# Performance work log

Hardware: AMD Instinct MI355X
Metric: run time of the kernel (lower is better)

Reference implementation:

```python
import jax, jax.numpy as jnp
import numpy as np

SIZE = 512  # context size
T, D1, D2 = 32768, 512, 512
HID = int(SIZE * 1.5)  # 768, units of the 'context_linear' Dense


def setup_inputs() -> dict:
    key = jax.random.key(0)
    ks = jax.random.split(key, 8)
    din = D1 + D2
    return {
        "x1": jax.random.normal(ks[0], (T, D1), jnp.float32),
        "x2": jax.random.normal(ks[1], (T, D2), jnp.float32),
        "context0": jax.random.normal(ks[2], (1, SIZE), jnp.float32) * 0.1,  # tf.Variable init stddev=0.1
        "W_linear": jax.random.normal(ks[3], (din, HID), jnp.float32) * 0.02,
        "b_linear": jnp.zeros((HID,), jnp.float32),
        "W_embed": jax.random.normal(ks[4], (HID, SIZE), jnp.float32) * 0.02,
        "W_rate": jax.random.normal(ks[5], (SIZE, 1), jnp.float32) * 0.02,
        "W_forget": jax.random.normal(ks[6], (SIZE, SIZE), jnp.float32) * 0.02,
    }


def reference(x1, x2, context0, W_linear, b_linear, W_embed, W_rate, W_forget):
    # z = embed(linear(concat(inputs))) : Dense(1.5*size, linear) -> Dense(size, sigmoid, no bias)
    z = jnp.concatenate([x1, x2], axis=-1)                      # [T, D1+D2]
    z = jax.nn.sigmoid((z @ W_linear + b_linear) @ W_embed)     # [T, SIZE]
    # rate gate depends only on z_t, so precompute it in one GEMM
    r = jnp.tanh(z @ W_rate)[:, 0]                              # [T]

    # recurrence: c_t = softmax(c_{t-1} @ Wf) * c_{t-1} + r_t * z_t
    def step(c, zr):
        zt, rt = zr
        f = jax.nn.softmax(c @ W_forget)                        # [SIZE]
        c_new = f * c + rt * zt
        return c_new, c_new

    _, ys = jax.lax.scan(step, context0[0], (z, r))             # ys: [T, SIZE]
    return ys
```

## Files before the change

### kernel.cpp

```cpp
#include <hip/hip_runtime.h>
#include <stdint.h>
#include <stddef.h>


typedef __attribute__((ext_vector_type(8))) short bf16x8;
typedef __attribute__((ext_vector_type(4))) float f32x4;

__device__ __forceinline__ unsigned short f32_to_bf16(float f) {
  union { float f; unsigned u; } v; v.f = f;
  unsigned u = v.u;
  return (unsigned short)((u + 0x7fffu + ((u >> 16) & 1u)) >> 16);
}
__device__ __forceinline__ float bf16_to_f32(unsigned short h) {
  union { unsigned u; float f; } v; v.u = ((unsigned)h) << 16; return v.f;
}

__device__ __forceinline__ unsigned char f32_to_e4m3(float f) {
  float a = fabsf(f);
  unsigned char s = (unsigned char)((__float_as_uint(f) >> 24) & 0x80u);
  if (a >= 448.0f) return s | 0x7Eu;
  if (a < 0.015625f) {
    unsigned m = (unsigned)rintf(a * 512.0f);
    return s | (unsigned char)m;
  }
  unsigned u = __float_as_uint(a);
  unsigned r = u + 0x7FFFFu + ((u >> 20) & 1u);
  unsigned e = (r >> 23) - 120u;
  unsigned m = (r >> 20) & 7u;
  if (e >= 16u) return s | 0x7Eu;
  return s | (unsigned char)((e << 3) | m);
}

__global__ void k_convert_x(const float* __restrict__ x1, const float* __restrict__ x2,
                            unsigned short* __restrict__ Xb) {
  int id = blockIdx.x * 256 + threadIdx.x;
  int t  = id >> 8;
  int c4 = (id & 255) * 4;
  float4 v;
  if (c4 < 512) v = *(const float4*)(x1 + (size_t)t * 512 + c4);
  else          v = *(const float4*)(x2 + (size_t)t * 512 + (c4 - 512));
  ushort4 o;
  o.x = f32_to_bf16(v.x); o.y = f32_to_bf16(v.y);
  o.z = f32_to_bf16(v.z); o.w = f32_to_bf16(v.w);
  *(ushort4*)(Xb + (size_t)t * 1024 + c4) = o;
}

__global__ void k_convert_w(const float* __restrict__ Wl, const float* __restrict__ We,
                            const float* __restrict__ Wf,
                            unsigned short* __restrict__ WlT, unsigned short* __restrict__ WeT,
                            unsigned char* __restrict__ Wf8) {
  int id = blockIdx.x * 256 + threadIdx.x;
  if (id < 786432) {
    int n = id >> 10, k = id & 1023;
    WlT[id] = f32_to_bf16(Wl[(size_t)k * 768 + n]);
  } else if (id < 1179648) {
    int j = id - 786432;
    int n = j / 768, k = j - n * 768;
    WeT[j] = f32_to_bf16(We[(size_t)k * 512 + n]);
  } else {
    int j = id - 1179648;
    int n = j >> 9, k = j & 511;
    Wf8[j] = f32_to_e4m3(Wf[(size_t)k * 512 + n] * 16.0f);
  }
}

template <int MODE>
__global__ void k_gemm_bt(const unsigned short* __restrict__ A,
                          const unsigned short* __restrict__ Bt,
                          const float* __restrict__ bias,
                          unsigned short* __restrict__ Cb,
                          float* __restrict__ Cf,
                          int M, int N, int K) {
  __shared__ unsigned short As[128 * 32];
  __shared__ unsigned short Bs[128 * 32];
  const int tid = threadIdx.x;
  const int wv = tid >> 6, lane = tid & 63;
  const int nb = N >> 7;
  const int bm = blockIdx.x / nb, bn = blockIdx.x % nb;
  const int wm = wv >> 1, wn = wv & 1;
  f32x4 acc[4][4];
#pragma unroll
  for (int i = 0; i < 4; ++i)
#pragma unroll
    for (int j = 0; j < 4; ++j) acc[i][j] = f32x4{0.f, 0.f, 0.f, 0.f};

  const unsigned short* Ag = A + (size_t)(bm * 128 + (tid >> 2)) * K + (tid & 3) * 8;
  const unsigned short* Bg = Bt + (size_t)(bn * 128 + (tid >> 2)) * K + (tid & 3) * 8;
  const int sidx = (tid >> 2) * 32 + (tid & 3) * 8;
  const int lm = lane & 15;
  const int qk = (lane >> 4) * 8;

  for (int k0 = 0; k0 < K; k0 += 32) {
    bf16x8 a0 = *(const bf16x8*)(Ag + k0);
    bf16x8 a1 = *(const bf16x8*)(Ag + k0 + (size_t)64 * K);
    bf16x8 b0 = *(const bf16x8*)(Bg + k0);
    bf16x8 b1 = *(const bf16x8*)(Bg + k0 + (size_t)64 * K);
    __syncthreads();
    *(bf16x8*)(As + sidx)        = a0;
    *(bf16x8*)(As + sidx + 2048) = a1;
    *(bf16x8*)(Bs + sidx)        = b0;
    *(bf16x8*)(Bs + sidx + 2048) = b1;
    __syncthreads();
    bf16x8 af[4], bfr[4];
#pragma unroll
    for (int mt = 0; mt < 4; ++mt)
      af[mt] = *(const bf16x8*)(As + (wm * 64 + mt * 16 + lm) * 32 + qk);
#pragma unroll
    for (int nt = 0; nt < 4; ++nt)
      bfr[nt] = *(const bf16x8*)(Bs + (wn * 64 + nt * 16 + lm) * 32 + qk);
#pragma unroll
    for (int mt = 0; mt < 4; ++mt)
#pragma unroll
      for (int nt = 0; nt < 4; ++nt)
        acc[mt][nt] = __builtin_amdgcn_mfma_f32_16x16x32_bf16(af[mt], bfr[nt], acc[mt][nt], 0, 0, 0);
  }

  const int row0 = bm * 128 + wm * 64 + (lane >> 4) * 4;
  const int col0 = bn * 128 + wn * 64 + lm;
#pragma unroll
  for (int mt = 0; mt < 4; ++mt)
#pragma unroll
    for (int nt = 0; nt < 4; ++nt)
#pragma unroll
      for (int rr = 0; rr < 4; ++rr) {
        int row = row0 + mt * 16 + rr;
        int col = col0 + nt * 16;
        float v = acc[mt][nt][rr];
        if (MODE == 0) {
          v += bias[col];
          Cb[(size_t)row * N + col] = f32_to_bf16(v);
        } else {
          v = 1.0f / (1.0f + __expf(-v));
          Cf[(size_t)row * N + col] = v;
        }
      }
}

__global__ void k_rate(const float* __restrict__ Z, const float* __restrict__ Wr,
                       float* __restrict__ r) {
  const int lane = threadIdx.x & 63;
  const int t = blockIdx.x * 4 + (threadIdx.x >> 6);
  const float4* z4 = (const float4*)(Z + (size_t)t * 512 + lane * 8);
  const float4* w4 = (const float4*)(Wr + lane * 8);
  float4 za = z4[0], zb = z4[1], wa = w4[0], wb = w4[1];
  float acc = za.x * wa.x + za.y * wa.y + za.z * wa.z + za.w * wa.w +
              zb.x * wb.x + zb.y * wb.y + zb.z * wb.z + zb.w * wb.w;
#pragma unroll
  for (int off = 32; off > 0; off >>= 1) acc += __shfl_down(acc, off, 64);
  if (lane == 0) r[t] = tanhf(acc);
}

__global__ __launch_bounds__(1024) void k_recur(
    const unsigned char* __restrict__ Wf8, const float* __restrict__ Z,
    const float* __restrict__ rArr, const float* __restrict__ ctx0,
    float* __restrict__ out) {
  __shared__ unsigned char Cq[16 * 520];
  __shared__ float Lg[16 * 516];

  const int tid = threadIdx.x;
  const int wv = tid >> 6;
  const int lane = tid & 63;
  const int lm = lane & 15;
  const int qk = (lane >> 4) * 8;

  long Bf[2][16];
  const int nbase = wv * 32;
#pragma unroll
  for (int nt = 0; nt < 2; ++nt)
#pragma unroll
    for (int kt = 0; kt < 16; ++kt)
      Bf[nt][kt] = *(const long*)(Wf8 + (size_t)(nbase + nt * 16 + lm) * 512 + kt * 32 + qk);

  const int g = wv;
  const int cg = blockIdx.x * 16 + g;
  const int colBase = lane * 8;
  float c[8];
  if (cg == 0) {
#pragma unroll
    for (int j = 0; j < 8; ++j) c[j] = ctx0[colBase + j];
  } else {
#pragma unroll
    for (int j = 0; j < 8; ++j) c[j] = 0.f;
  }
  {
    unsigned long long pk = 0;
#pragma unroll
    for (int j = 0; j < 8; ++j)
      pk |= (unsigned long long)f32_to_e4m3(c[j] * 16.0f) << (8 * j);
    *(unsigned long long*)(Cq + g * 520 + colBase) = pk;
  }
  __syncthreads();

  for (int s = 0; s < 12; ++s) {
    f32x4 acc0 = {0.f, 0.f, 0.f, 0.f}, acc1 = {0.f, 0.f, 0.f, 0.f};
#pragma unroll
    for (int kt = 0; kt < 16; ++kt) {
      long a = *(const long*)(Cq + lm * 520 + kt * 32 + qk);
      acc0 = __builtin_amdgcn_mfma_f32_16x16x32_fp8_fp8(a, Bf[0][kt], acc0, 0, 0, 0);
      acc1 = __builtin_amdgcn_mfma_f32_16x16x32_fp8_fp8(a, Bf[1][kt], acc1, 0, 0, 0);
    }
#pragma unroll
    for (int rr = 0; rr < 4; ++rr) {
      Lg[((lane >> 4) * 4 + rr) * 516 + nbase + lm]      = acc0[rr];
      Lg[((lane >> 4) * 4 + rr) * 516 + nbase + 16 + lm] = acc1[rr];
    }
    __syncthreads();

    float l[8];
    const float* lg = Lg + g * 516 + colBase;
#pragma unroll
    for (int j = 0; j < 8; ++j) l[j] = lg[j] * (1.0f / 256.0f);
    float m = l[0];
#pragma unroll
    for (int j = 1; j < 8; ++j) m = fmaxf(m, l[j]);
#pragma unroll
    for (int off = 1; off < 64; off <<= 1) m = fmaxf(m, __shfl_xor(m, off, 64));
    float sum = 0.f;
#pragma unroll
    for (int j = 0; j < 8; ++j) { l[j] = __expf(l[j] - m); sum += l[j]; }
#pragma unroll
    for (int off = 1; off < 64; off <<= 1) sum += __shfl_xor(sum, off, 64);
    const float inv = 1.0f / sum;

    const int t = cg * 8 - 4 + s;
    if (t >= 0) {
      const float4* z4 = (const float4*)(Z + (size_t)t * 512 + colBase);
      float4 za = z4[0], zb = z4[1];
      float zz[8] = {za.x, za.y, za.z, za.w, zb.x, zb.y, zb.z, zb.w};
      const float rt = rArr[t];
#pragma unroll
      for (int j = 0; j < 8; ++j)
        c[j] = l[j] * inv * c[j] + rt * zz[j];
      if (s >= 4) {
        float4 o0 = {c[0], c[1], c[2], c[3]};
        float4 o1 = {c[4], c[5], c[6], c[7]};
        *(float4*)(out + (size_t)t * 512 + colBase)     = o0;
        *(float4*)(out + (size_t)t * 512 + colBase + 4) = o1;
      }
    }
    unsigned long long pk = 0;
#pragma unroll
    for (int j = 0; j < 8; ++j)
      pk |= (unsigned long long)f32_to_e4m3(c[j] * 16.0f) << (8 * j);
    *(unsigned long long*)(Cq + g * 520 + colBase) = pk;
    __syncthreads();
  }
}

extern "C" void kernel_launch(void* const* d_in, const int* in_sizes, int n_in,
                              void* d_out, int out_size, void* d_ws, size_t ws_size,
                              hipStream_t stream) {
  const float* x1   = (const float*)d_in[0];
  const float* x2   = (const float*)d_in[1];
  const float* ctx0 = (const float*)d_in[2];
  const float* Wl   = (const float*)d_in[3];
  const float* bl   = (const float*)d_in[4];
  const float* We   = (const float*)d_in[5];
  const float* Wr   = (const float*)d_in[6];
  const float* Wf   = (const float*)d_in[7];
  float* out = (float*)d_out;

  char* ws = (char*)d_ws;
  if (ws_size < 120193024u) return;
  unsigned short* Xb  = (unsigned short*)(ws);
  float*          Z32 = (float*)(ws);
  unsigned short* WlT = (unsigned short*)(ws + 67108864);
  unsigned short* WeT = (unsigned short*)(ws + 68681728);
  unsigned char*  Wf8 = (unsigned char*) (ws + 69468160);
  float*          rb  = (float*)         (ws + 69730304);
  unsigned short* H   = (unsigned short*)(ws + 69861376);

  k_convert_x<<<32768, 256, 0, stream>>>(x1, x2, Xb);
  k_convert_w<<<5632, 256, 0, stream>>>(Wl, We, Wf, WlT, WeT, Wf8);
  k_gemm_bt<0><<<1536, 256, 0, stream>>>(Xb, WlT, bl, H, nullptr, 32768, 768, 1024);
  k_gemm_bt<1><<<1024, 256, 0, stream>>>(H, WeT, bl, nullptr, Z32, 32768, 512, 768);
  k_rate<<<8192, 256, 0, stream>>>(Z32, Wr, rb);
  k_recur<<<256, 1024, 0, stream>>>(Wf8, Z32, rb, ctx0, out);
}
```

Baseline: 382.2 us.

## Tile weight transpose, load GEMM tiles directly to LDS, remap blocks per XCD

The strided per-element weight conversion becomes a 32x32 shared-memory tiled transpose, so both reads and writes are coalesced. The GEMM now loads its tiles with global_load_lds, writing straight into LDS without staging through registers. Block indices are also remapped so that each XCD works on a contiguous band of M rows, which is meant to improve L2 reuse. The async LDS loads need no wait counter before the barrier to be correct, so there is a risk of a race if the barrier does not also wait for them.

```diff
diff --git a/kernel.cpp b/kernel.cpp
--- a/kernel.cpp
+++ b/kernel.cpp
@@ -10,9 +10,6 @@
   union { float f; unsigned u; } v; v.f = f;
   unsigned u = v.u;
   return (unsigned short)((u + 0x7fffu + ((u >> 16) & 1u)) >> 16);
-}
-__device__ __forceinline__ float bf16_to_f32(unsigned short h) {
-  union { unsigned u; float f; } v; v.u = ((unsigned)h) << 16; return v.f;
 }
 
 __device__ __forceinline__ unsigned char f32_to_e4m3(float f) {
@@ -29,6 +26,12 @@
   unsigned m = (r >> 20) & 7u;
   if (e >= 16u) return s | 0x7Eu;
   return s | (unsigned char)((e << 3) | m);
+}
+
+__device__ __forceinline__ void async16(const void* g, void* l) {
+  __builtin_amdgcn_global_load_lds(
+      (const __attribute__((address_space(1))) unsigned int*)g,
+      (__attribute__((address_space(3))) unsigned int*)l, 16, 0, 0);
 }
 
 __global__ void k_convert_x(const float* __restrict__ x1, const float* __restrict__ x2,
@@ -45,22 +48,30 @@
   *(ushort4*)(Xb + (size_t)t * 1024 + c4) = o;
 }
 
-__global__ void k_convert_w(const float* __restrict__ Wl, const float* __restrict__ We,
-                            const float* __restrict__ Wf,
-                            unsigned short* __restrict__ WlT, unsigned short* __restrict__ WeT,
-                            unsigned char* __restrict__ Wf8) {
-  int id = blockIdx.x * 256 + threadIdx.x;
-  if (id < 786432) {
-    int n = id >> 10, k = id & 1023;
-    WlT[id] = f32_to_bf16(Wl[(size_t)k * 768 + n]);
-  } else if (id < 1179648) {
-    int j = id - 786432;
-    int n = j / 768, k = j - n * 768;
-    WeT[j] = f32_to_bf16(We[(size_t)k * 512 + n]);
-  } else {
-    int j = id - 1179648;
-    int n = j >> 9, k = j & 511;
-    Wf8[j] = f32_to_e4m3(Wf[(size_t)k * 512 + n] * 16.0f);
+__global__ void k_transpose_w(const float* __restrict__ Wl, const float* __restrict__ We,
+                              const float* __restrict__ Wf,
+                              unsigned short* __restrict__ WlT,
+                              unsigned short* __restrict__ WeT,
+                              unsigned char* __restrict__ Wf8) {
+  __shared__ float tile[32][33];
+  int b = blockIdx.x;
+  const float* src; int C, R, tr, tc, mode;
+  if (b < 768)       { src = Wl; R = 1024; C = 768; tr = b / 24;  tc = b % 24;  mode = 0; }
+  else if (b < 1152) { int j = b - 768;  src = We; R = 768; C = 512; tr = j / 16; tc = j % 16; mode = 1; }
+  else               { int j = b - 1152; src = Wf; R = 512; C = 512; tr = j / 16; tc = j % 16; mode = 2; }
+  const int tx = threadIdx.x & 31, ty = threadIdx.x >> 5;
+  const int r0 = tr * 32, c0 = tc * 32;
+#pragma unroll
+  for (int p = 0; p < 4; ++p)
+    tile[ty + p * 8][tx] = src[(size_t)(r0 + ty + p * 8) * C + c0 + tx];
+  __syncthreads();
+#pragma unroll
+  for (int p = 0; p < 4; ++p) {
+    int n = c0 + ty + p * 8;
+    float v = tile[tx][ty + p * 8];
+    if (mode == 0)      WlT[(size_t)n * 1024 + r0 + tx] = f32_to_bf16(v);
+    else if (mode == 1) WeT[(size_t)n * 768  + r0 + tx] = f32_to_bf16(v);
+    else                Wf8[(size_t)n * 512  + r0 + tx] = f32_to_e4m3(v * 16.0f);
   }
 }
 
@@ -76,7 +87,10 @@
   const int tid = threadIdx.x;
   const int wv = tid >> 6, lane = tid & 63;
   const int nb = N >> 7;
-  const int bm = blockIdx.x / nb, bn = blockIdx.x % nb;
+  const int xcd = blockIdx.x & 7;
+  const int s   = blockIdx.x >> 3;
+  const int bm  = xcd * (M >> 10) + s / nb;
+  const int bn  = s % nb;
   const int wm = wv >> 1, wn = wv & 1;
   f32x4 acc[4][4];
 #pragma unroll
@@ -86,20 +100,17 @@
 
   const unsigned short* Ag = A + (size_t)(bm * 128 + (tid >> 2)) * K + (tid & 3) * 8;
   const unsigned short* Bg = Bt + (size_t)(bn * 128 + (tid >> 2)) * K + (tid & 3) * 8;
-  const int sidx = (tid >> 2) * 32 + (tid & 3) * 8;
+  unsigned short* AsW = As + wv * 512;
+  unsigned short* BsW = Bs + wv * 512;
   const int lm = lane & 15;
   const int qk = (lane >> 4) * 8;
 
   for (int k0 = 0; k0 < K; k0 += 32) {
-    bf16x8 a0 = *(const bf16x8*)(Ag + k0);
-    bf16x8 a1 = *(const bf16x8*)(Ag + k0 + (size_t)64 * K);
-    bf16x8 b0 = *(const bf16x8*)(Bg + k0);
-    bf16x8 b1 = *(const bf16x8*)(Bg + k0 + (size_t)64 * K);
-    __syncthreads();
-    *(bf16x8*)(As + sidx)        = a0;
-    *(bf16x8*)(As + sidx + 2048) = a1;
-    *(bf16x8*)(Bs + sidx)        = b0;
-    *(bf16x8*)(Bs + sidx + 2048) = b1;
+    __syncthreads();
+    async16(Ag + k0,                  AsW);
+    async16(Ag + k0 + (size_t)64 * K, AsW + 2048);
+    async16(Bg + k0,                  BsW);
+    async16(Bg + k0 + (size_t)64 * K, BsW + 2048);
     __syncthreads();
     bf16x8 af[4], bfr[4];
 #pragma unroll
@@ -271,7 +282,7 @@
   unsigned short* H   = (unsigned short*)(ws + 69861376);
 
   k_convert_x<<<32768, 256, 0, stream>>>(x1, x2, Xb);
-  k_convert_w<<<5632, 256, 0, stream>>>(Wl, We, Wf, WlT, WeT, Wf8);
+  k_transpose_w<<<1408, 256, 0, stream>>>(Wl, We, Wf, WlT, WeT, Wf8);
   k_gemm_bt<0><<<1536, 256, 0, stream>>>(Xb, WlT, bl, H, nullptr, 32768, 768, 1024);
   k_gemm_bt<1><<<1024, 256, 0, stream>>>(H, WeT, bl, nullptr, Z32, 32768, 512, 768);
   k_rate<<<8192, 256, 0, stream>>>(Z32, Wr, rb);
```

After: 356.7 us. 6.7% less time.
